# Kernel optimization log

Measured on AMD Instinct MI355X. Metric: run time of the kernel, lower is better.

Reference implementation:

```python
import jax, jax.numpy as jnp
import numpy as np

B, T, E = 4, 2048, 256
H = 8
HD = E // H
FE = 4
L = 4
EPS = 1e-5


def _layernorm(x, g, b):
    mu = jnp.mean(x, axis=-1, keepdims=True)
    var = jnp.mean((x - mu) ** 2, axis=-1, keepdims=True)
    return (x - mu) * jax.lax.rsqrt(var + EPS) * g + b


def setup_inputs() -> dict:
    key = jax.random.key(0)
    ks = jax.random.split(key, 14)
    s = 0.02
    inp = {
        "x": jax.random.normal(ks[0], (B, T, E), dtype=jnp.float32),
        "qkv_w": jax.random.normal(ks[1], (L, E, 3 * E), dtype=jnp.float32) * s,
        "qkv_b": jnp.zeros((L, 3 * E), jnp.float32),
        "out_w": jax.random.normal(ks[2], (L, E, E), dtype=jnp.float32) * s,
        "out_b": jnp.zeros((L, E), jnp.float32),
        "ff1_w": jax.random.normal(ks[3], (L, E, FE * E), dtype=jnp.float32) * s,
        "ff1_b": jnp.zeros((L, FE * E), jnp.float32),
        "ff2_w": jax.random.normal(ks[4], (L, FE * E, E), dtype=jnp.float32) * s,
        "ff2_b": jnp.zeros((L, E), jnp.float32),
        "ln1_g": jnp.ones((L, E), jnp.float32),
        "ln1_b": jnp.zeros((L, E), jnp.float32),
        "ln2_g": jnp.ones((L, E), jnp.float32),
        "ln2_b": jnp.zeros((L, E), jnp.float32),
    }
    return inp


def _fourier_pe(x):
    # freqs over even indices: 10000^(-i/E), i = 0,2,...,E-2  -> E/2 freqs
    freqs = jnp.power(10000.0, -jnp.arange(0, E, 2, dtype=jnp.float32) / E)
    pos = jnp.arange(T, dtype=jnp.float32)[:, None]          # (T,1)
    sinusoid = pos * freqs[None, :]                            # (T, E/2)
    pe = jnp.concatenate([jnp.sin(sinusoid), jnp.cos(sinusoid)], axis=-1)  # (T,E)
    return x + pe[None, :, :]


def _forward(x, qkv_w, qkv_b, out_w, out_b, ff1_w, ff1_b, ff2_w, ff2_b,
             ln1_g, ln1_b, ln2_g, ln2_b):
    x = _fourier_pe(x)
    scale = 1.0 / np.sqrt(HD)
    for i in range(L):
        # attention (dropout = identity at eval)
        qkv = x @ qkv_w[i] + qkv_b[i]                          # (B,T,3E)
        qkv = qkv.reshape(B, T, H, 3, HD)                      # chunk of 3*hd -> (3,hd)
        q, k, v = qkv[..., 0, :], qkv[..., 1, :], qkv[..., 2, :]  # (B,T,H,HD)
        scores = jnp.einsum("bqhd,bkhd->bhqk", q, k) * scale   # (B,H,T,T)
        w = jax.nn.softmax(scores, axis=-1)
        attn = jnp.einsum("bhqk,bkhd->bqhd", w, v).reshape(B, T, E)
        attn = attn @ out_w[i] + out_b[i]
        x = _layernorm(x + attn, ln1_g[i], ln1_b[i])
        # feedforward
        h = jax.nn.relu(x @ ff1_w[i] + ff1_b[i])
        ff = h @ ff2_w[i] + ff2_b[i]
        x = _layernorm(x + ff, ln2_g[i], ln2_b[i])
    return x


def reference(x, qkv_w, qkv_b, out_w, out_b, ff1_w, ff1_b, ff2_w, ff2_b,
              ln1_g, ln1_b, ln2_g, ln2_b):
    return _forward(x, qkv_w, qkv_b, out_w, out_b, ff1_w, ff1_b, ff2_w, ff2_b,
                    ln1_g, ln1_b, ln2_g, ln2_b)
```

## Files before the change

### kernel.cpp

```cpp
#include <hip/hip_runtime.h>
#include <hip/hip_bf16.h>
#include <stdint.h>

typedef unsigned short u16;
typedef _Float16 f16;
typedef short vs8 __attribute__((ext_vector_type(8)));
typedef float vf4 __attribute__((ext_vector_type(4)));
typedef _Float16 vh2 __attribute__((ext_vector_type(2)));
typedef _Float16 vh4 __attribute__((ext_vector_type(4)));
typedef _Float16 vh8 __attribute__((ext_vector_type(8)));
typedef __fp16 hw2 __attribute__((ext_vector_type(2)));


__device__ __forceinline__ void gload16(const u16* g, u16* l) {
  __builtin_amdgcn_global_load_lds((const __attribute__((address_space(1))) void*)g,
                                   (__attribute__((address_space(3))) void*)l,
                                   16, 0, 0);
}

__device__ __forceinline__ float fexp2(float x) {
#if __has_builtin(__builtin_amdgcn_exp2f)
  return __builtin_amdgcn_exp2f(x);
#else
  return __expf(x * 0.69314718056f);
#endif
}

__global__ void pe_trans_all(
    const float* __restrict__ x, __hip_bfloat16* __restrict__ Xb,
    const float* __restrict__ w0, const float* __restrict__ w1,
    const float* __restrict__ w2, const float* __restrict__ w3,
    u16* __restrict__ o0, u16* __restrict__ o1,
    u16* __restrict__ o2, u16* __restrict__ o3) {
  __shared__ float tile[32][33];
  int bid = blockIdx.x;
  int tid = threadIdx.x;
  if (bid < 2048) {
    int gid = bid * 256 + tid;
    int row = gid >> 6;
    int e0 = (gid & 63) * 4;
    int t = row & 2047;
    int f0 = (e0 < 128) ? e0 : (e0 - 128);
    const float c = -13.287712379549449f / 128.0f;
    const float inv2pi = 0.15915494309189535f;
    float4 xv = *(const float4*)(x + (size_t)row * 256 + e0);
    u16 o[4];
#pragma unroll
    for (int j = 0; j < 4; ++j) {
      float freq = fexp2(c * (float)(f0 + j));
      float rev = (float)t * freq * inv2pi;
      rev = rev - floorf(rev);
      float pe = (e0 < 128) ? __builtin_amdgcn_sinf(rev) : __builtin_amdgcn_cosf(rev);
      float xin = (j == 0) ? xv.x : (j == 1) ? xv.y : (j == 2) ? xv.z : xv.w;
      __hip_bfloat16 hb = __float2bfloat16(xin + pe);
      o[j] = *(u16*)&hb;
    }
    *(uint2*)((u16*)Xb + (size_t)row * 256 + e0) = *(uint2*)o;
  } else {
    int flat = bid - 2048;
    int layer = flat / 768;
    int r = flat - layer * 768;
    const float* ip; u16* op; int K, N, kt, nt;
    if (r < 192)      {              ip = w0; op = o0; K = 256;  N = 768;  kt = r & 7;  nt = r >> 3; }
    else if (r < 256) { int q=r-192; ip = w1; op = o1; K = 256;  N = 256;  kt = q & 7;  nt = q >> 3; }
    else if (r < 512) { int q=r-256; ip = w2; op = o2; K = 256;  N = 1024; kt = q & 7;  nt = q >> 3; }
    else              { int q=r-512; ip = w3; op = o3; K = 1024; N = 256;  kt = q & 31; nt = q >> 5; }
    ip += (size_t)layer * K * N;
    op += (size_t)layer * N * K;
    int k0 = kt * 32, n0 = nt * 32;
    int tx = tid & 31, ty = tid >> 5;
#pragma unroll
    for (int rr = 0; rr < 4; ++rr) {
      int k = ty + rr * 8;
      tile[k][tx] = ip[(size_t)(k0 + k) * N + (n0 + tx)];
    }
    __syncthreads();
#pragma unroll
    for (int rr = 0; rr < 4; ++rr) {
      int n = ty + rr * 8;
      __hip_bfloat16 v = __float2bfloat16(tile[tx][n]);
      op[(size_t)(n0 + n) * K + (k0 + tx)] = *(u16*)&v;
    }
  }
}

__global__ __launch_bounds__(256, 2) void gemm_relu(
    const u16* __restrict__ A, const u16* __restrict__ Bt,
    const float* __restrict__ bias, __hip_bfloat16* __restrict__ outB,
    int M, int N, int K) {
  __shared__ u16 As[128 * 64];
  __shared__ u16 Bs[128 * 64];
  int tid = threadIdx.x;
  int wave = tid >> 6, lane = tid & 63;
  int wm = wave & 1, wn = wave >> 1;
  int flat = blockIdx.x + blockIdx.y * 8;
  int logical = (flat & 7) * 64 + (flat >> 3);
  int m0 = (logical >> 3) * 128, n0 = (logical & 7) * 128;
  int lr = lane & 15, lq = lane >> 4;
  int swz = (lr & 7) << 3;

  vf4 acc[4][4];
#pragma unroll
  for (int i = 0; i < 4; ++i)
#pragma unroll
    for (int j = 0; j < 4; ++j) {
      acc[i][j][0] = 0.f; acc[i][j][1] = 0.f; acc[i][j][2] = 0.f; acc[i][j][3] = 0.f;
    }

  int srow = tid >> 3;
  int sc = (tid & 7) * 8;
  int cswz = (((tid & 7) ^ (srow & 7)) * 8);
  const u16* ag = A + (size_t)(m0 + srow) * K + cswz;
  const u16* bg = Bt + (size_t)(n0 + srow) * K + cswz;
  u16* al = As + srow * 64 + sc;
  u16* bl = Bs + srow * 64 + sc;
  const size_t rstride32 = (size_t)32 * K;

  for (int k0 = 0; k0 < K; k0 += 64) {
#pragma unroll
    for (int r = 0; r < 4; ++r) {
      gload16(ag + k0 + r * rstride32, al + r * 32 * 64);
      gload16(bg + k0 + r * rstride32, bl + r * 32 * 64);
    }
    __syncthreads();
#pragma unroll
    for (int kk = 0; kk < 2; ++kk) {
      vs8 av[4], bv[4];
#pragma unroll
      for (int i = 0; i < 4; ++i)
        av[i] = *(const vs8*)&As[(wm * 64 + i * 16 + lr) * 64 + ((kk * 32 + lq * 8) ^ swz)];
#pragma unroll
      for (int j = 0; j < 4; ++j)
        bv[j] = *(const vs8*)&Bs[(wn * 64 + j * 16 + lr) * 64 + ((kk * 32 + lq * 8) ^ swz)];
#pragma unroll
      for (int i = 0; i < 4; ++i)
#pragma unroll
        for (int j = 0; j < 4; ++j)
          acc[i][j] = __builtin_amdgcn_mfma_f32_16x16x32_bf16(av[i], bv[j], acc[i][j], 0, 0, 0);
    }
    __syncthreads();
  }

#pragma unroll
  for (int i = 0; i < 4; ++i) {
    int row0 = m0 + wm * 64 + i * 16 + lq * 4;
#pragma unroll
    for (int j = 0; j < 4; ++j) {
      int col = n0 + wn * 64 + j * 16 + lr;
      float bb = bias[col];
#pragma unroll
      for (int r = 0; r < 4; ++r) {
        size_t idx = (size_t)(row0 + r) * N + col;
        outB[idx] = __float2bfloat16(fmaxf(acc[i][j][r] + bb, 0.0f));
      }
    }
  }
}

__global__ __launch_bounds__(256, 3) void gemm_qkv64(
    const u16* __restrict__ A, const u16* __restrict__ Bt,
    const float* __restrict__ bias, f16* __restrict__ outH,
    int M, int N, int K) {
  __shared__ u16 As[64 * 64];
  __shared__ u16 Bs[128 * 64];
  int tid = threadIdx.x;
  int wave = tid >> 6, lane = tid & 63;
  int wm = wave & 1, wn = wave >> 1;
  int flat = blockIdx.x + blockIdx.y * 6;
  int logical = (flat & 7) * 96 + (flat >> 3);
  int ly = logical / 6, lx = logical - ly * 6;
  int m0 = ly * 64, n0 = lx * 128;
  int lr = lane & 15, lq = lane >> 4;
  int swz = (lr & 7) << 3;

  vf4 acc[2][4];
#pragma unroll
  for (int i = 0; i < 2; ++i)
#pragma unroll
    for (int j = 0; j < 4; ++j) { acc[i][j][0]=0.f; acc[i][j][1]=0.f; acc[i][j][2]=0.f; acc[i][j][3]=0.f; }

  int srow = tid >> 3;
  int sc = (tid & 7) * 8;
  int cswz = (((tid & 7) ^ (srow & 7)) * 8);
  const u16* ag = A + (size_t)(m0 + srow) * K + cswz;
  const u16* bg = Bt + (size_t)(n0 + srow) * K + cswz;
  u16* al = As + srow * 64 + sc;
  u16* bl = Bs + srow * 64 + sc;
  const size_t rstride32 = (size_t)32 * K;

  for (int k0 = 0; k0 < K; k0 += 64) {
#pragma unroll
    for (int r = 0; r < 2; ++r)
      gload16(ag + k0 + r * rstride32, al + r * 32 * 64);
#pragma unroll
    for (int r = 0; r < 4; ++r)
      gload16(bg + k0 + r * rstride32, bl + r * 32 * 64);
    __syncthreads();
#pragma unroll
    for (int kk = 0; kk < 2; ++kk) {
      vs8 av[2], bv[4];
#pragma unroll
      for (int i = 0; i < 2; ++i)
        av[i] = *(const vs8*)&As[(wm * 32 + i * 16 + lr) * 64 + ((kk * 32 + lq * 8) ^ swz)];
#pragma unroll
      for (int j = 0; j < 4; ++j)
        bv[j] = *(const vs8*)&Bs[(wn * 64 + j * 16 + lr) * 64 + ((kk * 32 + lq * 8) ^ swz)];
#pragma unroll
      for (int i = 0; i < 2; ++i)
#pragma unroll
        for (int j = 0; j < 4; ++j)
          acc[i][j] = __builtin_amdgcn_mfma_f32_16x16x32_bf16(av[i], bv[j], acc[i][j], 0, 0, 0);
    }
    __syncthreads();
  }

#pragma unroll
  for (int i = 0; i < 2; ++i) {
    int row0 = m0 + wm * 32 + i * 16 + lq * 4;
#pragma unroll
    for (int j = 0; j < 4; ++j) {
      int col = n0 + wn * 64 + j * 16 + lr;
      float bb = bias[col];
#pragma unroll
      for (int r = 0; r < 4; ++r)
        outH[(size_t)(row0 + r) * N + col] = (f16)(acc[i][j][r] + bb);
    }
  }
}

__global__ __launch_bounds__(256, 2) void gemm_ln(
    const u16* __restrict__ A, const u16* __restrict__ Bt,
    const float* __restrict__ bias, const __hip_bfloat16* __restrict__ res,
    const float* __restrict__ gam, const float* __restrict__ bet,
    __hip_bfloat16* __restrict__ outB, float* __restrict__ outF, int K,
    const f16* __restrict__ OfA, const float* __restrict__ lf) {
  __shared__ u16 As[16 * 64];
  __shared__ u16 Bs[256 * 64];
  __shared__ float ps[4][16], ps2[4][16], mur[16], rsr[16];
  __shared__ float invs[8][16];
  int tid = threadIdx.x;
  int wave = tid >> 6, lane = tid & 63;
  int wn = wave;
  int lr = lane & 15, lq = lane >> 4;
  int m0 = blockIdx.x * 16;
  int swz = (lr & 7) << 3;

  vf4 acc[4];
#pragma unroll
  for (int j = 0; j < 4; ++j) { acc[j][0]=0.f; acc[j][1]=0.f; acc[j][2]=0.f; acc[j][3]=0.f; }

  int srA = tid >> 3;
  int scA = (tid & 7) * 8;
  int cswzA = (((tid & 7) ^ (srA & 7)) * 8);
  const u16* ag = A + (size_t)(m0 + srA) * K + cswzA;
  u16* al = As + srA * 64 + scA;
  const u16* bg = Bt + (size_t)srA * K + cswzA;
  u16* bl = Bs + srA * 64 + scA;

  if (OfA) {
    if (tid < 128) {
      int h = tid >> 4, rl = tid & 15;
      int row = m0 + rl, bb_ = row >> 11, t = row & 2047;
      int g = bb_ * 8 + h;
      invs[h][rl] = 1.0f / (lf[g * 2048 + t] + lf[65536 + g * 2048 + t]);
    }
    __syncthreads();
  }

  for (int k0 = 0; k0 < K; k0 += 64) {
    if (tid < 128) {
      if (OfA) {
        size_t off = (size_t)(m0 + srA) * 256 + k0 + cswzA;
        vh8 a0 = *(const vh8*)(OfA + off);
        vh8 a1 = *(const vh8*)(OfA + 2097152 + off);
        float inv = invs[(k0 + cswzA) >> 5][srA];
        union { vs8 v; u16 u[8]; } pk;
#pragma unroll
        for (int j = 0; j < 8; ++j) {
          __hip_bfloat16 hb = __float2bfloat16(((float)a0[j] + (float)a1[j]) * inv);
          pk.u[j] = *(u16*)&hb;
        }
        *(vs8*)al = pk.v;
      } else {
        gload16(ag + k0, al);
      }
    }
#pragma unroll
    for (int r = 0; r < 8; ++r)
      gload16(bg + k0 + (size_t)(r * 32) * K, bl + r * 32 * 64);
    __syncthreads();
#pragma unroll
    for (int kk = 0; kk < 2; ++kk) {
      vs8 av, bv[4];
      av = *(const vs8*)&As[lr * 64 + ((kk * 32 + lq * 8) ^ swz)];
#pragma unroll
      for (int j = 0; j < 4; ++j)
        bv[j] = *(const vs8*)&Bs[(wn * 64 + j * 16 + lr) * 64 + ((kk * 32 + lq * 8) ^ swz)];
#pragma unroll
      for (int j = 0; j < 4; ++j)
        acc[j] = __builtin_amdgcn_mfma_f32_16x16x32_bf16(av, bv[j], acc[j], 0, 0, 0);
    }
    __syncthreads();
  }

  float sum_[4], sq_[4];
#pragma unroll
  for (int r = 0; r < 4; ++r) { sum_[r] = 0.f; sq_[r] = 0.f; }
#pragma unroll
  for (int j = 0; j < 4; ++j) {
    int col = wn * 64 + j * 16 + lr;
    float bb = bias[col];
#pragma unroll
    for (int r = 0; r < 4; ++r) {
      int row = m0 + lq * 4 + r;
      float v = acc[j][r] + bb + __bfloat162float(res[(size_t)row * 256 + col]);
      acc[j][r] = v;
      sum_[r] += v;
      sq_[r] += v * v;
    }
  }
#pragma unroll
  for (int r = 0; r < 4; ++r) {
#pragma unroll
    for (int m = 1; m <= 8; m <<= 1) {
      sum_[r] += __shfl_xor(sum_[r], m);
      sq_[r]  += __shfl_xor(sq_[r], m);
    }
  }
  if (lr == 0) {
#pragma unroll
    for (int r = 0; r < 4; ++r) {
      int rl = lq * 4 + r;
      ps[wn][rl] = sum_[r];
      ps2[wn][rl] = sq_[r];
    }
  }
  __syncthreads();
  if (tid < 16) {
    float s = ps[0][tid] + ps[1][tid] + ps[2][tid] + ps[3][tid];
    float s2 = ps2[0][tid] + ps2[1][tid] + ps2[2][tid] + ps2[3][tid];
    float mu = s * (1.0f / 256.0f);
    float var = s2 * (1.0f / 256.0f) - mu * mu;
    mur[tid] = mu;
    rsr[tid] = rsqrtf(var + 1e-5f);
  }
  __syncthreads();
#pragma unroll
  for (int r = 0; r < 4; ++r) {
    int rl = lq * 4 + r;
    float mu = mur[rl], rs = rsr[rl];
    int row = m0 + rl;
#pragma unroll
    for (int j = 0; j < 4; ++j) {
      int col = wn * 64 + j * 16 + lr;
      float o = (acc[j][r] - mu) * rs * gam[col] + bet[col];
      size_t idx = (size_t)row * 256 + col;
      outB[idx] = __float2bfloat16(o);
      if (outF) outF[idx] = o;
    }
  }
}

__global__ __launch_bounds__(512, 4) void attn_mfma(const f16* __restrict__ qkv,
                                                    f16* __restrict__ Of,
                                                    float* __restrict__ lf) {
  __shared__ __align__(16) u16 lds[2][9344];
  int tid = threadIdx.x;
  int wave = tid >> 6, lane = tid & 63;
  int lr = lane & 15, quad = lane >> 4;

  int id = blockIdx.x;
  int xcd = id & 7, slot = id >> 3;
  int grp = xcd * 4 + (slot & 3);
  int qt = (slot >> 2) & 7;
  int split = slot >> 5;
  int b = grp >> 3, h = grp & 7;
  int q0 = qt * 256;
  int kv0 = split << 10;
  int rowbase = b * 2048;
  const f16* base_bh = qkv + (size_t)rowbase * 768 + h * 96;

  vh8 qf[2];
#pragma unroll
  for (int nt = 0; nt < 2; ++nt) {
    int qr = q0 + wave * 32 + nt * 16 + lr;
    vh8 t = *(const vh8*)(base_bh + (size_t)qr * 768 + quad * 8);
#pragma unroll
    for (int j = 0; j < 8; ++j) t[j] = t[j] * (f16)0.25508682f;
    qf[nt] = t;
  }

  vf4 O[2][2], lO[2];
#pragma unroll
  for (int a = 0; a < 2; ++a) {
    lO[a][0]=0.f; lO[a][1]=0.f; lO[a][2]=0.f; lO[a][3]=0.f;
#pragma unroll
    for (int d = 0; d < 2; ++d) { O[a][d][0]=0.f; O[a][d][1]=0.f; O[a][d][2]=0.f; O[a][d][3]=0.f; }
  }

  int srK = tid >> 2;
  int scK = (tid & 3) * 8;
  const f16* kg = base_bh + (size_t)(kv0 + srK) * 768 + 32 + scK;
  int kvp = tid >> 3;
  int d4 = (tid & 7) * 4;
  const f16* vg = base_bh + (size_t)(kv0 + kvp * 2) * 768 + 64 + d4;

  const vf4 z4 = {0.f, 0.f, 0.f, 0.f};
  const vh4 onesh = {(f16)1.0f, (f16)1.0f, (f16)1.0f, (f16)1.0f};
  const size_t cstep = (size_t)128 * 768;

  {
    vh8 k0 = *(const vh8*)kg;
    *(vh8*)&lds[0][srK * 40 + scK] = k0;
    vh4 a = *(const vh4*)vg;
    vh4 bb = *(const vh4*)(vg + 768);
    f16* vt0 = (f16*)&lds[0][5120];
#pragma unroll
    for (int i = 0; i < 4; ++i) {
      vh2 pr; pr[0] = a[i]; pr[1] = bb[i];
      *(vh2*)(vt0 + (d4 + i) * 132 + kvp * 2) = pr;
    }
  }
  __syncthreads();

  for (int c = 0; c < 8; ++c) {
    int cur = c & 1;
    const f16* Ks = (const f16*)&lds[cur][0];
    const f16* VT = (const f16*)&lds[cur][5120];

    vh8 kn; vh4 va, vb;
    if (c < 7) {
      kn = *(const vh8*)(kg + (size_t)(c + 1) * cstep);
      const f16* vp = vg + (size_t)(c + 1) * cstep;
      va = *(const vh4*)vp;
      vb = *(const vh4*)(vp + 768);
    }

    __builtin_amdgcn_s_setprio(1);
#pragma unroll
    for (int t16 = 0; t16 < 8; ++t16) {
      vh8 ak = *(const vh8*)&Ks[(t16 * 16 + lr) * 40 + quad * 8];
      vf4 s0 = __builtin_amdgcn_mfma_f32_16x16x32_f16(ak, qf[0], z4, 0, 0, 0);
      vf4 s1 = __builtin_amdgcn_mfma_f32_16x16x32_f16(ak, qf[1], z4, 0, 0, 0);
      vh4 p0, p1;
      ((hw2*)&p0)[0] = __builtin_amdgcn_cvt_pkrtz(fexp2(s0[0]), fexp2(s0[1]));
      ((hw2*)&p0)[1] = __builtin_amdgcn_cvt_pkrtz(fexp2(s0[2]), fexp2(s0[3]));
      ((hw2*)&p1)[0] = __builtin_amdgcn_cvt_pkrtz(fexp2(s1[0]), fexp2(s1[1]));
      ((hw2*)&p1)[1] = __builtin_amdgcn_cvt_pkrtz(fexp2(s1[2]), fexp2(s1[3]));
      vh4 vf0 = *(const vh4*)&VT[(0 * 16 + lr) * 132 + t16 * 16 + quad * 4];
      vh4 vf1 = *(const vh4*)&VT[(1 * 16 + lr) * 132 + t16 * 16 + quad * 4];
      O[0][0] = __builtin_amdgcn_mfma_f32_16x16x16f16(p0, vf0, O[0][0], 0, 0, 0);
      O[0][1] = __builtin_amdgcn_mfma_f32_16x16x16f16(p0, vf1, O[0][1], 0, 0, 0);
      O[1][0] = __builtin_amdgcn_mfma_f32_16x16x16f16(p1, vf0, O[1][0], 0, 0, 0);
      O[1][1] = __builtin_amdgcn_mfma_f32_16x16x16f16(p1, vf1, O[1][1], 0, 0, 0);
      lO[0] = __builtin_amdgcn_mfma_f32_16x16x16f16(p0, onesh, lO[0], 0, 0, 0);
      lO[1] = __builtin_amdgcn_mfma_f32_16x16x16f16(p1, onesh, lO[1], 0, 0, 0);
    }
    __builtin_amdgcn_s_setprio(0);

    if (c < 7) {
      *(vh8*)&lds[cur ^ 1][srK * 40 + scK] = kn;
      f16* vt1 = (f16*)&lds[cur ^ 1][5120];
#pragma unroll
      for (int i = 0; i < 4; ++i) {
        vh2 pr; pr[0] = va[i]; pr[1] = vb[i];
        *(vh2*)(vt1 + (d4 + i) * 132 + kvp * 2) = pr;
      }
    }
    __syncthreads();
  }

#pragma unroll
  for (int nt = 0; nt < 2; ++nt) {
#pragma unroll
    for (int r = 0; r < 4; ++r) {
      int tq = q0 + wave * 32 + nt * 16 + quad * 4 + r;
      if (lr == 0) lf[split * 65536 + grp * 2048 + tq] = lO[nt][r];
      int row = rowbase + tq;
#pragma unroll
      for (int dt = 0; dt < 2; ++dt) {
        int col = h * 32 + dt * 16 + lr;
        Of[(size_t)split * 2097152 + (size_t)row * 256 + col] = (f16)O[nt][dt][r];
      }
    }
  }
}

extern "C" void kernel_launch(void* const* d_in, const int* in_sizes, int n_in,
                              void* d_out, int out_size, void* d_ws, size_t ws_size,
                              hipStream_t stream) {
  (void)in_sizes; (void)n_in; (void)out_size; (void)ws_size;
  const float* x     = (const float*)d_in[0];
  const float* qkv_b = (const float*)d_in[2];
  const float* out_b = (const float*)d_in[4];
  const float* ff1_b = (const float*)d_in[6];
  const float* ff2_b = (const float*)d_in[8];
  const float* ln1_g = (const float*)d_in[9];
  const float* ln1_b = (const float*)d_in[10];
  const float* ln2_g = (const float*)d_in[11];
  const float* ln2_b = (const float*)d_in[12];

  char* ws = (char*)d_ws;
  f16*            Of    = (f16*)(ws + 0);
  __hip_bfloat16* Xb    = (__hip_bfloat16*)(ws + 8388608);
  float*          lf    = (float*)(ws + 12582912);
  f16*            qkvH  = (f16*)(ws + 25165824);
  __hip_bfloat16* hB    = (__hip_bfloat16*)(ws + 20971520);
  u16* qkvwT = (u16*)(ws + 37748736);
  u16* outwT = (u16*)(ws + 39321600);
  u16* ff1wT = (u16*)(ws + 39845888);
  u16* ff2wT = (u16*)(ws + 41943040);

  pe_trans_all<<<5120, 256, 0, stream>>>(x, Xb,
      (const float*)d_in[1], (const float*)d_in[3], (const float*)d_in[5], (const float*)d_in[7],
      qkvwT, outwT, ff1wT, ff2wT);

  for (int l = 0; l < 4; ++l) {
    gemm_qkv64<<<dim3(6, 128), 256, 0, stream>>>((const u16*)Xb, qkvwT + (size_t)l * 768 * 256,
        qkv_b + l * 768, qkvH, 8192, 768, 256);
    attn_mfma<<<512, 512, 0, stream>>>(qkvH, Of, lf);
    gemm_ln<<<512, 256, 0, stream>>>(nullptr, outwT + (size_t)l * 256 * 256,
        out_b + l * 256, Xb, ln1_g + l * 256, ln1_b + l * 256, Xb, nullptr, 256, Of, lf);
    gemm_relu<<<dim3(8, 64), 256, 0, stream>>>((const u16*)Xb, ff1wT + (size_t)l * 1024 * 256,
        ff1_b + l * 1024, hB, 8192, 1024, 256);
    float* lnout = (l == 3) ? (float*)d_out : nullptr;
    gemm_ln<<<512, 256, 0, stream>>>((const u16*)hB, ff2wT + (size_t)l * 256 * 1024,
        ff2_b + l * 256, Xb, ln2_g + l * 256, ln2_b + l * 256, Xb, lnout, 1024, nullptr, nullptr);
  }
}
```

Measured before the change: 401.8 us.

## Drop split-KV attention and normalize output inside attention kernel

Attention blocks now process the full key range in 16 chunks instead of two halves, so each block divides by its own row sum and writes bf16 output directly. The out-projection GEMM loses its combine step and loads A via async global-to-LDS like the other GEMMs. This removes the partial-output and row-sum buffers and their extra traffic, at the cost of halving the attention grid to 256 blocks, which reduces parallelism and latency hiding.

Result: no change. 404.8 us (+0.7%).

```diff
diff --git a/kernel.cpp b/kernel.cpp
--- a/kernel.cpp
+++ b/kernel.cpp
@@ -232,12 +232,10 @@
     const u16* __restrict__ A, const u16* __restrict__ Bt,
     const float* __restrict__ bias, const __hip_bfloat16* __restrict__ res,
     const float* __restrict__ gam, const float* __restrict__ bet,
-    __hip_bfloat16* __restrict__ outB, float* __restrict__ outF, int K,
-    const f16* __restrict__ OfA, const float* __restrict__ lf) {
+    __hip_bfloat16* __restrict__ outB, float* __restrict__ outF, int K) {
   __shared__ u16 As[16 * 64];
   __shared__ u16 Bs[256 * 64];
   __shared__ float ps[4][16], ps2[4][16], mur[16], rsr[16];
-  __shared__ float invs[8][16];
   int tid = threadIdx.x;
   int wave = tid >> 6, lane = tid & 63;
   int wn = wave;
@@ -257,34 +255,8 @@
   const u16* bg = Bt + (size_t)srA * K + cswzA;
   u16* bl = Bs + srA * 64 + scA;
 
-  if (OfA) {
-    if (tid < 128) {
-      int h = tid >> 4, rl = tid & 15;
-      int row = m0 + rl, bb_ = row >> 11, t = row & 2047;
-      int g = bb_ * 8 + h;
-      invs[h][rl] = 1.0f / (lf[g * 2048 + t] + lf[65536 + g * 2048 + t]);
-    }
-    __syncthreads();
-  }
-
   for (int k0 = 0; k0 < K; k0 += 64) {
-    if (tid < 128) {
-      if (OfA) {
-        size_t off = (size_t)(m0 + srA) * 256 + k0 + cswzA;
-        vh8 a0 = *(const vh8*)(OfA + off);
-        vh8 a1 = *(const vh8*)(OfA + 2097152 + off);
-        float inv = invs[(k0 + cswzA) >> 5][srA];
-        union { vs8 v; u16 u[8]; } pk;
-#pragma unroll
-        for (int j = 0; j < 8; ++j) {
-          __hip_bfloat16 hb = __float2bfloat16(((float)a0[j] + (float)a1[j]) * inv);
-          pk.u[j] = *(u16*)&hb;
-        }
-        *(vs8*)al = pk.v;
-      } else {
-        gload16(ag + k0, al);
-      }
-    }
+    if (tid < 128) gload16(ag + k0, al);
 #pragma unroll
     for (int r = 0; r < 8; ++r)
       gload16(bg + k0 + (size_t)(r * 32) * K, bl + r * 32 * 64);
@@ -362,8 +334,7 @@
 }
 
 __global__ __launch_bounds__(512, 4) void attn_mfma(const f16* __restrict__ qkv,
-                                                    f16* __restrict__ Of,
-                                                    float* __restrict__ lf) {
+                                                    __hip_bfloat16* __restrict__ out) {
   __shared__ __align__(16) u16 lds[2][9344];
   int tid = threadIdx.x;
   int wave = tid >> 6, lane = tid & 63;
@@ -372,11 +343,9 @@
   int id = blockIdx.x;
   int xcd = id & 7, slot = id >> 3;
   int grp = xcd * 4 + (slot & 3);
-  int qt = (slot >> 2) & 7;
-  int split = slot >> 5;
+  int qt = slot >> 2;
   int b = grp >> 3, h = grp & 7;
   int q0 = qt * 256;
-  int kv0 = split << 10;
   int rowbase = b * 2048;
   const f16* base_bh = qkv + (size_t)rowbase * 768 + h * 96;
 
@@ -400,10 +369,10 @@
 
   int srK = tid >> 2;
   int scK = (tid & 3) * 8;
-  const f16* kg = base_bh + (size_t)(kv0 + srK) * 768 + 32 + scK;
+  const f16* kg = base_bh + (size_t)srK * 768 + 32 + scK;
   int kvp = tid >> 3;
   int d4 = (tid & 7) * 4;
-  const f16* vg = base_bh + (size_t)(kv0 + kvp * 2) * 768 + 64 + d4;
+  const f16* vg = base_bh + (size_t)(kvp * 2) * 768 + 64 + d4;
 
   const vf4 z4 = {0.f, 0.f, 0.f, 0.f};
   const vh4 onesh = {(f16)1.0f, (f16)1.0f, (f16)1.0f, (f16)1.0f};
@@ -423,13 +392,13 @@
   }
   __syncthreads();
 
-  for (int c = 0; c < 8; ++c) {
+  for (int c = 0; c < 16; ++c) {
     int cur = c & 1;
     const f16* Ks = (const f16*)&lds[cur][0];
     const f16* VT = (const f16*)&lds[cur][5120];
 
     vh8 kn; vh4 va, vb;
-    if (c < 7) {
+    if (c < 15) {
       kn = *(const vh8*)(kg + (size_t)(c + 1) * cstep);
       const f16* vp = vg + (size_t)(c + 1) * cstep;
       va = *(const vh4*)vp;
@@ -458,7 +427,7 @@
     }
     __builtin_amdgcn_s_setprio(0);
 
-    if (c < 7) {
+    if (c < 15) {
       *(vh8*)&lds[cur ^ 1][srK * 40 + scK] = kn;
       f16* vt1 = (f16*)&lds[cur ^ 1][5120];
 #pragma unroll
@@ -474,13 +443,12 @@
   for (int nt = 0; nt < 2; ++nt) {
 #pragma unroll
     for (int r = 0; r < 4; ++r) {
-      int tq = q0 + wave * 32 + nt * 16 + quad * 4 + r;
-      if (lr == 0) lf[split * 65536 + grp * 2048 + tq] = lO[nt][r];
-      int row = rowbase + tq;
+      float inv = 1.0f / lO[nt][r];
+      int row = rowbase + q0 + wave * 32 + nt * 16 + quad * 4 + r;
 #pragma unroll
       for (int dt = 0; dt < 2; ++dt) {
         int col = h * 32 + dt * 16 + lr;
-        Of[(size_t)split * 2097152 + (size_t)row * 256 + col] = (f16)O[nt][dt][r];
+        out[(size_t)row * 256 + col] = __float2bfloat16(O[nt][dt][r] * inv);
       }
     }
   }
@@ -501,9 +469,8 @@
   const float* ln2_b = (const float*)d_in[12];
 
   char* ws = (char*)d_ws;
-  f16*            Of    = (f16*)(ws + 0);
+  __hip_bfloat16* attnB = (__hip_bfloat16*)(ws + 0);
   __hip_bfloat16* Xb    = (__hip_bfloat16*)(ws + 8388608);
-  float*          lf    = (float*)(ws + 12582912);
   f16*            qkvH  = (f16*)(ws + 25165824);
   __hip_bfloat16* hB    = (__hip_bfloat16*)(ws + 20971520);
   u16* qkvwT = (u16*)(ws + 37748736);
@@ -518,13 +485,13 @@
   for (int l = 0; l < 4; ++l) {
     gemm_qkv64<<<dim3(6, 128), 256, 0, stream>>>((const u16*)Xb, qkvwT + (size_t)l * 768 * 256,
         qkv_b + l * 768, qkvH, 8192, 768, 256);
-    attn_mfma<<<512, 512, 0, stream>>>(qkvH, Of, lf);
-    gemm_ln<<<512, 256, 0, stream>>>(nullptr, outwT + (size_t)l * 256 * 256,
-        out_b + l * 256, Xb, ln1_g + l * 256, ln1_b + l * 256, Xb, nullptr, 256, Of, lf);
+    attn_mfma<<<256, 512, 0, stream>>>(qkvH, attnB);
+    gemm_ln<<<512, 256, 0, stream>>>((const u16*)attnB, outwT + (size_t)l * 256 * 256,
+        out_b + l * 256, Xb, ln1_g + l * 256, ln1_b + l * 256, Xb, nullptr, 256);
     gemm_relu<<<dim3(8, 64), 256, 0, stream>>>((const u16*)Xb, ff1wT + (size_t)l * 1024 * 256,
         ff1_b + l * 1024, hB, 8192, 1024, 256);
     float* lnout = (l == 3) ? (float*)d_out : nullptr;
     gemm_ln<<<512, 256, 0, stream>>>((const u16*)hB, ff2wT + (size_t)l * 256 * 1024,
-        ff2_b + l * 256, Xb, ln2_g + l * 256, ln2_b + l * 256, Xb, lnout, 1024, nullptr, nullptr);
-  }
-}
+        ff2_b + l * 256, Xb, ln2_g + l * 256, ln2_b + l * 256, Xb, lnout, 1024);
+  }
+}
```
